# Optimization experiments

Measured on AMD Instinct MI355X. Metric: run time of the kernel, lower is better.

Reference implementation:

```python
import jax, jax.numpy as jnp
import numpy as np

BATCH, SEQ, DIM = 4, 4096, 1024


def setup_inputs() -> dict:
    key = jax.random.key(0)
    ks = jax.random.split(key, 7)
    return {
        "x": jax.random.normal(ks[0], (BATCH, SEQ, DIM), dtype=jnp.float32),
        "phazor_re": jax.random.normal(ks[1], (DIM,), dtype=jnp.float32),
        "phazor_im": jax.random.normal(ks[2], (DIM,), dtype=jnp.float32),
        "phazor_init_re": jax.random.normal(ks[3], (DIM,), dtype=jnp.float32),
        "phazor_init_im": jax.random.normal(ks[4], (DIM,), dtype=jnp.float32),
        "last_conv_re": jax.random.normal(ks[5], (BATCH, DIM), dtype=jnp.float32),
        "last_conv_im": jax.random.normal(ks[6], (BATCH, DIM), dtype=jnp.float32),
    }


def reference(x, phazor_re, phazor_im, phazor_init_re, phazor_init_im,
              last_conv_re, last_conv_im):
    L = x.shape[1]
    phazor_p = phazor_re + 1j * phazor_im                      # raw param (dim,)
    phazor_init = phazor_init_re + 1j * phazor_init_im          # (dim,)
    last_conv = last_conv_re + 1j * last_conv_im                # (batch, dim)

    mag = jnp.abs(phazor_p)
    phazor = phazor_p / mag * jnp.exp(-mag)                     # (dim,) |phazor|<1
    t = jnp.arange(L)[:, None]                                  # (L,1)
    phazor_prog = jnp.power(phazor[None, :], t)                 # (L, dim) = phazor^t
    filt = phazor_prog * phazor_init[None, :]                   # (L, dim)

    filt_fft = jnp.fft.fft(filt, n=2 * L, axis=0)               # (2L, dim)
    x_fft = jnp.fft.fft(x.astype(jnp.complex64), n=2 * L, axis=1)  # (B, 2L, dim)
    conv = jnp.fft.ifft(filt_fft[None] * x_fft, axis=1)[:, :L]  # (B, L, dim)

    # add decayed initial state: last_conv * phazor^(t+1)
    conv = conv + last_conv[:, None, :] * phazor_prog[None] * phazor[None, None, :]
    return conv.real
```

## Files before the change

### kernel.cpp

```cpp
#include <hip/hip_runtime.h>


#define BB 4
#define LL 4096
#define DD 1024
#define CHUNK 16
#define KK 256
#define SEG 32
#define NSEG 8

__device__ __forceinline__ void phazor_of(float pr, float pi, float& ar, float& ai) {
    float mag = sqrtf(pr * pr + pi * pi);
    float s = expf(-mag) / mag;
    ar = pr * s;
    ai = pi * s;
}

__device__ __forceinline__ void csq(float& r, float& i) {
    float nr = r * r - i * i;
    i = 2.f * r * i;
    r = nr;
}

__global__ __launch_bounds__(256, 4) void spiral_p1(
    const float* __restrict__ x,
    const float* __restrict__ p_re, const float* __restrict__ p_im,
    const float* __restrict__ in_re, const float* __restrict__ in_im,
    float2* __restrict__ S)
{
    int tid = blockIdx.x * 256 + threadIdx.x;
    int dq = tid & (DD / 4 - 1);
    int k  = (tid >> 8) & (KK - 1);
    int b  = tid >> 16;
    int d0 = dq * 4;

    float4 prv = *(const float4*)(p_re + d0);
    float4 piv = *(const float4*)(p_im + d0);
    float4 brv = *(const float4*)(in_re + d0);
    float4 biv = *(const float4*)(in_im + d0);
    float ar[4], ai[4];
    float br[4] = {brv.x, brv.y, brv.z, brv.w};
    float bi[4] = {biv.x, biv.y, biv.z, biv.w};
    {
        float prs[4] = {prv.x, prv.y, prv.z, prv.w};
        float pis[4] = {piv.x, piv.y, piv.z, piv.w};
#pragma unroll
        for (int q = 0; q < 4; ++q) phazor_of(prs[q], pis[q], ar[q], ai[q]);
    }

    float sr[4] = {0.f, 0.f, 0.f, 0.f};
    float si[4] = {0.f, 0.f, 0.f, 0.f};
    const float* xp = x + ((size_t)(b * LL + k * CHUNK) * DD + d0);

#pragma unroll
    for (int t0 = 0; t0 < CHUNK; t0 += 8) {
        float4 xv[8];
#pragma unroll
        for (int j = 0; j < 8; ++j)
            xv[j] = *(const float4*)(xp + (size_t)(t0 + j) * DD);
#pragma unroll
        for (int j = 0; j < 8; ++j) {
            float xs[4] = {xv[j].x, xv[j].y, xv[j].z, xv[j].w};
#pragma unroll
            for (int q = 0; q < 4; ++q) {
                float nr = fmaf(ar[q], sr[q], fmaf(-ai[q], si[q], br[q] * xs[q]));
                float ni = fmaf(ar[q], si[q], fmaf( ai[q], sr[q], bi[q] * xs[q]));
                sr[q] = nr; si[q] = ni;
            }
        }
    }

    float4* Sp = (float4*)(S + ((size_t)(b * KK + k) * DD + d0));
    Sp[0] = make_float4(sr[0], si[0], sr[1], si[1]);
    Sp[1] = make_float4(sr[2], si[2], sr[3], si[3]);
}

__global__ __launch_bounds__(128) void spiral_p2a(
    const float* __restrict__ p_re, const float* __restrict__ p_im,
    const float2* __restrict__ S,
    float2* __restrict__ R, float2* __restrict__ T)
{
    int gt  = blockIdx.x * 128 + threadIdx.x;
    int d   = gt & (DD - 1);
    int seg = (gt >> 10) & (NSEG - 1);
    int bb  = gt >> 13;

    float qr, qi;
    phazor_of(p_re[d], p_im[d], qr, qi);
#pragma unroll
    for (int i = 0; i < 4; ++i) csq(qr, qi);

    const int kk0 = seg * SEG;
    const float2* Sc = S + ((size_t)bb * KK * DD + d);
    float2*       Rc = R + ((size_t)bb * KK * DD + d);

    float2 buf[8];
#pragma unroll
    for (int j = 0; j < 8; ++j) buf[j] = Sc[(size_t)(kk0 + j) * DD];

    float cr = 0.f, ci = 0.f;
    for (int i = 0; i < SEG; i += 8) {
#pragma unroll
        for (int j = 0; j < 8; ++j) {
            Rc[(size_t)(kk0 + i + j) * DD] = make_float2(cr, ci);
            float2 s = buf[j];
            int kn = i + j + 8;
            buf[j] = Sc[(size_t)(kk0 + (kn < SEG ? kn : SEG - 1)) * DD];
            float nr = fmaf(qr, cr, fmaf(-qi, ci, s.x));
            float ni = fmaf(qr, ci, fmaf( qi, cr, s.y));
            cr = nr; ci = ni;
        }
    }
    T[((size_t)bb * NSEG + seg) * DD + d] = make_float2(cr, ci);
}

__global__ __launch_bounds__(256, 4) void spiral_p3(
    const float* __restrict__ x,
    const float* __restrict__ p_re, const float* __restrict__ p_im,
    const float* __restrict__ in_re, const float* __restrict__ in_im,
    const float* __restrict__ lc_re, const float* __restrict__ lc_im,
    const float2* __restrict__ R, const float2* __restrict__ T,
    float* __restrict__ out)
{
    int tid = blockIdx.x * 256 + threadIdx.x;
    int dq = tid & (DD / 4 - 1);
    int k  = (tid >> 8) & (KK - 1);
    int b  = tid >> 16;
    int d0 = dq * 4;
    int rel = k & (SEG - 1);
    int seg = k >> 5;

    float4 prv = *(const float4*)(p_re + d0);
    float4 piv = *(const float4*)(p_im + d0);
    float4 brv = *(const float4*)(in_re + d0);
    float4 biv = *(const float4*)(in_im + d0);
    float ar[4], ai[4];
    float br[4] = {brv.x, brv.y, brv.z, brv.w};
    float bi[4] = {biv.x, biv.y, biv.z, biv.w};
    {
        float prs[4] = {prv.x, prv.y, prv.z, prv.w};
        float pis[4] = {piv.x, piv.y, piv.z, piv.w};
#pragma unroll
        for (int q = 0; q < 4; ++q) phazor_of(prs[q], pis[q], ar[q], ai[q]);
    }

    float gr[4], gi[4];
    {
        float4 lrv = *(const float4*)(lc_re + b * DD + d0);
        float4 liv = *(const float4*)(lc_im + b * DD + d0);
        gr[0] = lrv.x; gr[1] = lrv.y; gr[2] = lrv.z; gr[3] = lrv.w;
        gi[0] = liv.x; gi[1] = liv.y; gi[2] = liv.z; gi[3] = liv.w;
        float Qr[4], Qi[4];
#pragma unroll
        for (int q = 0; q < 4; ++q) {
            Qr[q] = ar[q]; Qi[q] = ai[q];
#pragma unroll
            for (int i = 0; i < 9; ++i) csq(Qr[q], Qi[q]);
        }
        for (int s = 0; s < seg; ++s) {
            const float2* Tp = T + ((size_t)(b * NSEG + s) * DD + d0);
#pragma unroll
            for (int q = 0; q < 4; ++q) {
                float2 t = Tp[q];
                float nr = fmaf(Qr[q], gr[q], fmaf(-Qi[q], gi[q], t.x));
                float ni = fmaf(Qr[q], gi[q], fmaf( Qi[q], gr[q], t.y));
                gr[q] = nr; gi[q] = ni;
            }
        }
    }

    float cr[4], ci[4];
    {
        const float2* Rp = R + ((size_t)(b * KK + k) * DD + d0);
#pragma unroll
        for (int q = 0; q < 4; ++q) {
            float qdr = ar[q], qdi = ai[q];
#pragma unroll
            for (int i = 0; i < 4; ++i) csq(qdr, qdi);
            float pr = 1.f, pi = 0.f;
            float bpr = qdr, bpi = qdi;
#pragma unroll
            for (int bit = 0; bit < 5; ++bit) {
                if ((rel >> bit) & 1) {
                    float nr = pr * bpr - pi * bpi;
                    pi = pr * bpi + pi * bpr;
                    pr = nr;
                }
                csq(bpr, bpi);
            }
            float2 r = Rp[q];
            cr[q] = r.x + pr * gr[q] - pi * gi[q];
            ci[q] = r.y + pr * gi[q] + pi * gr[q];
        }
    }

    const size_t base = (size_t)(b * LL + k * CHUNK) * DD + d0;
    const float* xp = x + base;
    float* op = out + base;

#pragma unroll
    for (int t0 = 0; t0 < CHUNK; t0 += 8) {
        float4 xv[8];
#pragma unroll
        for (int j = 0; j < 8; ++j)
            xv[j] = *(const float4*)(xp + (size_t)(t0 + j) * DD);
#pragma unroll
        for (int j = 0; j < 8; ++j) {
            float xs[4] = {xv[j].x, xv[j].y, xv[j].z, xv[j].w};
            float os[4];
#pragma unroll
            for (int q = 0; q < 4; ++q) {
                float nr = fmaf(ar[q], cr[q], fmaf(-ai[q], ci[q], br[q] * xs[q]));
                float ni = fmaf(ar[q], ci[q], fmaf( ai[q], cr[q], bi[q] * xs[q]));
                cr[q] = nr; ci[q] = ni;
                os[q] = nr;
            }
            *(float4*)(op + (size_t)(t0 + j) * DD) = make_float4(os[0], os[1], os[2], os[3]);
        }
    }
}

extern "C" void kernel_launch(void* const* d_in, const int* in_sizes, int n_in,
                              void* d_out, int out_size, void* d_ws, size_t ws_size,
                              hipStream_t stream) {
    const float* x      = (const float*)d_in[0];
    const float* p_re   = (const float*)d_in[1];
    const float* p_im   = (const float*)d_in[2];
    const float* pin_re = (const float*)d_in[3];
    const float* pin_im = (const float*)d_in[4];
    const float* lc_re  = (const float*)d_in[5];
    const float* lc_im  = (const float*)d_in[6];
    float* out = (float*)d_out;

    char* ws = (char*)d_ws;
    float2* S = (float2*)(ws);
    float2* R = (float2*)(ws + (size_t)8  * 1024 * 1024);
    float2* T = (float2*)(ws + (size_t)16 * 1024 * 1024);

    spiral_p1 <<<dim3(1024), dim3(256), 0, stream>>>(x, p_re, p_im, pin_re, pin_im, S);
    spiral_p2a<<<dim3(256),  dim3(128), 0, stream>>>(p_re, p_im, S, R, T);
    spiral_p3 <<<dim3(1024), dim3(256), 0, stream>>>(x, p_re, p_im, pin_re, pin_im,
                                                     lc_re, lc_im, R, T, out);
}
```

Before: 140.8 us.

## Precompute per-segment carry in separate kernel and prefetch x early in p3

Adds a small spiral_p2b kernel that scans the segment totals once per (batch, dim) and writes the carry-in state for each segment. This removes the serial loop over up to seven segments with nine complex squarings that every thread in spiral_p3 used to run. spiral_p3 now issues its x, R and Gseg loads at the top so memory latency overlaps the phazor-power math, and splits the 16-step loop into two explicit halves. The cost is one extra tiny kernel launch and higher register pressure from holding more prefetched data.

Result: no change. 141.6 us (+0.6%).

```diff
diff --git a/kernel.cpp b/kernel.cpp
--- a/kernel.cpp
+++ b/kernel.cpp
@@ -114,12 +114,43 @@
     T[((size_t)bb * NSEG + seg) * DD + d] = make_float2(cr, ci);
 }
 
+__global__ __launch_bounds__(256) void spiral_p2b(
+    const float* __restrict__ p_re, const float* __restrict__ p_im,
+    const float* __restrict__ lc_re, const float* __restrict__ lc_im,
+    const float2* __restrict__ T,
+    float2* __restrict__ Gseg)
+{
+    int tid = blockIdx.x * 256 + threadIdx.x;
+    int d = tid & (DD - 1);
+    int b = tid >> 10;
+
+    float2 tv[NSEG];
+#pragma unroll
+    for (int s = 0; s < NSEG; ++s)
+        tv[s] = T[((size_t)(b * NSEG + s)) * DD + d];
+
+    float gr = lc_re[b * DD + d];
+    float gi = lc_im[b * DD + d];
+
+    float Qr, Qi;
+    phazor_of(p_re[d], p_im[d], Qr, Qi);
+#pragma unroll
+    for (int i = 0; i < 9; ++i) csq(Qr, Qi);
+
+#pragma unroll
+    for (int s = 0; s < NSEG; ++s) {
+        Gseg[((size_t)(b * NSEG + s)) * DD + d] = make_float2(gr, gi);
+        float nr = fmaf(Qr, gr, fmaf(-Qi, gi, tv[s].x));
+        float ni = fmaf(Qr, gi, fmaf( Qi, gr, tv[s].y));
+        gr = nr; gi = ni;
+    }
+}
+
 __global__ __launch_bounds__(256, 4) void spiral_p3(
     const float* __restrict__ x,
     const float* __restrict__ p_re, const float* __restrict__ p_im,
     const float* __restrict__ in_re, const float* __restrict__ in_im,
-    const float* __restrict__ lc_re, const float* __restrict__ lc_im,
-    const float2* __restrict__ R, const float2* __restrict__ T,
+    const float2* __restrict__ R, const float2* __restrict__ Gseg,
     float* __restrict__ out)
 {
     int tid = blockIdx.x * 256 + threadIdx.x;
@@ -130,10 +161,29 @@
     int rel = k & (SEG - 1);
     int seg = k >> 5;
 
+    const size_t base = (size_t)(b * LL + k * CHUNK) * DD + d0;
+    const float* xp = x + base;
+
+    float4 xlo[8];
+#pragma unroll
+    for (int j = 0; j < 8; ++j)
+        xlo[j] = *(const float4*)(xp + (size_t)j * DD);
+
+    float2 rv[4], gs[4];
+    {
+        const float2* Rp = R    + ((size_t)(b * KK   + k  ) * DD + d0);
+        const float2* Gp = Gseg + ((size_t)(b * NSEG + seg) * DD + d0);
+#pragma unroll
+        for (int q = 0; q < 4; ++q) rv[q] = Rp[q];
+#pragma unroll
+        for (int q = 0; q < 4; ++q) gs[q] = Gp[q];
+    }
+
     float4 prv = *(const float4*)(p_re + d0);
     float4 piv = *(const float4*)(p_im + d0);
     float4 brv = *(const float4*)(in_re + d0);
     float4 biv = *(const float4*)(in_im + d0);
+
     float ar[4], ai[4];
     float br[4] = {brv.x, brv.y, brv.z, brv.w};
     float bi[4] = {biv.x, biv.y, biv.z, biv.w};
@@ -144,34 +194,8 @@
         for (int q = 0; q < 4; ++q) phazor_of(prs[q], pis[q], ar[q], ai[q]);
     }
 
-    float gr[4], gi[4];
-    {
-        float4 lrv = *(const float4*)(lc_re + b * DD + d0);
-        float4 liv = *(const float4*)(lc_im + b * DD + d0);
-        gr[0] = lrv.x; gr[1] = lrv.y; gr[2] = lrv.z; gr[3] = lrv.w;
-        gi[0] = liv.x; gi[1] = liv.y; gi[2] = liv.z; gi[3] = liv.w;
-        float Qr[4], Qi[4];
-#pragma unroll
-        for (int q = 0; q < 4; ++q) {
-            Qr[q] = ar[q]; Qi[q] = ai[q];
-#pragma unroll
-            for (int i = 0; i < 9; ++i) csq(Qr[q], Qi[q]);
-        }
-        for (int s = 0; s < seg; ++s) {
-            const float2* Tp = T + ((size_t)(b * NSEG + s) * DD + d0);
-#pragma unroll
-            for (int q = 0; q < 4; ++q) {
-                float2 t = Tp[q];
-                float nr = fmaf(Qr[q], gr[q], fmaf(-Qi[q], gi[q], t.x));
-                float ni = fmaf(Qr[q], gi[q], fmaf( Qi[q], gr[q], t.y));
-                gr[q] = nr; gi[q] = ni;
-            }
-        }
-    }
-
     float cr[4], ci[4];
     {
-        const float2* Rp = R + ((size_t)(b * KK + k) * DD + d0);
 #pragma unroll
         for (int q = 0; q < 4; ++q) {
             float qdr = ar[q], qdi = ai[q];
@@ -188,35 +212,42 @@
                 }
                 csq(bpr, bpi);
             }
-            float2 r = Rp[q];
-            cr[q] = r.x + pr * gr[q] - pi * gi[q];
-            ci[q] = r.y + pr * gi[q] + pi * gr[q];
-        }
-    }
-
-    const size_t base = (size_t)(b * LL + k * CHUNK) * DD + d0;
-    const float* xp = x + base;
+            cr[q] = rv[q].x + pr * gs[q].x - pi * gs[q].y;
+            ci[q] = rv[q].y + pr * gs[q].y + pi * gs[q].x;
+        }
+    }
+
+    float4 xhi[8];
+#pragma unroll
+    for (int j = 0; j < 8; ++j)
+        xhi[j] = *(const float4*)(xp + (size_t)(8 + j) * DD);
+
     float* op = out + base;
-
-#pragma unroll
-    for (int t0 = 0; t0 < CHUNK; t0 += 8) {
-        float4 xv[8];
-#pragma unroll
-        for (int j = 0; j < 8; ++j)
-            xv[j] = *(const float4*)(xp + (size_t)(t0 + j) * DD);
-#pragma unroll
-        for (int j = 0; j < 8; ++j) {
-            float xs[4] = {xv[j].x, xv[j].y, xv[j].z, xv[j].w};
-            float os[4];
-#pragma unroll
-            for (int q = 0; q < 4; ++q) {
-                float nr = fmaf(ar[q], cr[q], fmaf(-ai[q], ci[q], br[q] * xs[q]));
-                float ni = fmaf(ar[q], ci[q], fmaf( ai[q], cr[q], bi[q] * xs[q]));
-                cr[q] = nr; ci[q] = ni;
-                os[q] = nr;
-            }
-            *(float4*)(op + (size_t)(t0 + j) * DD) = make_float4(os[0], os[1], os[2], os[3]);
-        }
+#pragma unroll
+    for (int j = 0; j < 8; ++j) {
+        float xs[4] = {xlo[j].x, xlo[j].y, xlo[j].z, xlo[j].w};
+        float os[4];
+#pragma unroll
+        for (int q = 0; q < 4; ++q) {
+            float nr = fmaf(ar[q], cr[q], fmaf(-ai[q], ci[q], br[q] * xs[q]));
+            float ni = fmaf(ar[q], ci[q], fmaf( ai[q], cr[q], bi[q] * xs[q]));
+            cr[q] = nr; ci[q] = ni;
+            os[q] = nr;
+        }
+        *(float4*)(op + (size_t)j * DD) = make_float4(os[0], os[1], os[2], os[3]);
+    }
+#pragma unroll
+    for (int j = 0; j < 8; ++j) {
+        float xs[4] = {xhi[j].x, xhi[j].y, xhi[j].z, xhi[j].w};
+        float os[4];
+#pragma unroll
+        for (int q = 0; q < 4; ++q) {
+            float nr = fmaf(ar[q], cr[q], fmaf(-ai[q], ci[q], br[q] * xs[q]));
+            float ni = fmaf(ar[q], ci[q], fmaf( ai[q], cr[q], bi[q] * xs[q]));
+            cr[q] = nr; ci[q] = ni;
+            os[q] = nr;
+        }
+        *(float4*)(op + (size_t)(8 + j) * DD) = make_float4(os[0], os[1], os[2], os[3]);
     }
 }
 
@@ -233,12 +264,14 @@
     float* out = (float*)d_out;
 
     char* ws = (char*)d_ws;
-    float2* S = (float2*)(ws);
-    float2* R = (float2*)(ws + (size_t)8  * 1024 * 1024);
-    float2* T = (float2*)(ws + (size_t)16 * 1024 * 1024);
+    float2* S    = (float2*)(ws);
+    float2* R    = (float2*)(ws + (size_t)8  * 1024 * 1024);
+    float2* T    = (float2*)(ws + (size_t)16 * 1024 * 1024);
+    float2* Gseg = (float2*)(ws + (size_t)16 * 1024 * 1024 + 256 * 1024);
 
     spiral_p1 <<<dim3(1024), dim3(256), 0, stream>>>(x, p_re, p_im, pin_re, pin_im, S);
     spiral_p2a<<<dim3(256),  dim3(128), 0, stream>>>(p_re, p_im, S, R, T);
+    spiral_p2b<<<dim3(16),   dim3(256), 0, stream>>>(p_re, p_im, lc_re, lc_im, T, Gseg);
     spiral_p3 <<<dim3(1024), dim3(256), 0, stream>>>(x, p_re, p_im, pin_re, pin_im,
-                                                     lc_re, lc_im, R, T, out);
-}
+                                                     R, Gseg, out);
+}
```
